# Optimization experiments

Hardware: AMD Instinct MI355X
Metric: run time of the kernel (lower is better)

The kernel has to match this reference:

```python
import jax, jax.numpy as jnp
import numpy as np
from jax import lax

B, T, U, H, INNER, V = 4, 200, 100, 320, 512, 1000
BLANK = 0


def setup_inputs() -> dict:
    key = jax.random.key(0)
    ks = jax.random.split(key, 8)
    enc_state = jax.random.normal(ks[0], (B, T, H), dtype=jnp.float32)
    dec_state = jax.random.normal(ks[1], (B, U + 1, H), dtype=jnp.float32)
    tokens = jax.random.randint(ks[2], (B, U), 1, V, dtype=jnp.int32)
    output_length = jnp.full((B,), T, dtype=jnp.int32)
    tokens_length = jnp.full((B,), U, dtype=jnp.int32)
    s1 = 1.0 / np.sqrt(2 * H)
    s2 = 1.0 / np.sqrt(INNER)
    W1 = jax.random.uniform(ks[3], (2 * H, INNER), minval=-s1, maxval=s1, dtype=jnp.float32)
    b1 = jax.random.uniform(ks[4], (INNER,), minval=-s1, maxval=s1, dtype=jnp.float32)
    W2 = jax.random.uniform(ks[5], (INNER, V), minval=-s2, maxval=s2, dtype=jnp.float32)
    b2 = jax.random.uniform(ks[6], (V,), minval=-s2, maxval=s2, dtype=jnp.float32)
    return {"enc_state": enc_state, "dec_state": dec_state, "tokens": tokens,
            "output_length": output_length, "tokens_length": tokens_length,
            "W1": W1, "b1": b1, "W2": W2, "b2": b2}


def joint_logits(enc_state, dec_state, W1, b1, W2, b2):
    # concat joint: cat(enc[b,t], dec[b,u]) @ W1 == enc @ W1[:H] + dec @ W1[H:]
    h_enc = jnp.einsum('bth,hi->bti', enc_state, W1[:H])      # (B,T,INNER)
    h_dec = jnp.einsum('buh,hi->bui', dec_state, W1[H:])      # (B,U+1,INNER)
    h = jnp.tanh(h_enc[:, :, None, :] + h_dec[:, None, :, :] + b1)  # (B,T,U+1,INNER)
    return jnp.einsum('btui,iv->btuv', h, W2) + b2            # (B,T,U+1,V)


def rnnt_loss(log_probs, tokens, output_length, tokens_length):
    # log_probs: (B,T,U+1,V); tokens: (B,U) int
    Bn, Tn, U1, _ = log_probs.shape
    blank_lp = log_probs[..., BLANK]                           # (B,T,U+1)
    label_lp = jnp.take_along_axis(
        log_probs[:, :, :U1 - 1, :],
        tokens[:, None, :, None].astype(jnp.int32).repeat(Tn, axis=1),
        axis=-1)[..., 0]                                       # (B,T,U)

    # row t=0: alpha[0,u] = sum_{u'<u} label_lp[0,u']
    def row0_step(c, a):
        n = c + a
        return n, n
    init0 = jnp.zeros((Bn,), dtype=log_probs.dtype)
    _, rest0 = lax.scan(row0_step, init0, label_lp[:, 0, :].T)  # (U,B)
    alpha0 = jnp.concatenate([init0[None], rest0], axis=0).T    # (B,U+1)

    def t_step(alpha_prev, xs):
        blank_prev, label_t = xs                # (B,U+1), (B,U)
        b = alpha_prev + blank_prev             # blank transition from row t-1
        def u_step(c, inp):
            b_u, a_prev = inp
            n = jnp.logaddexp(b_u, c + a_prev)
            return n, n
        first = b[:, 0]
        _, rest = lax.scan(u_step, first, (b[:, 1:].T, label_t.T))
        alpha_t = jnp.concatenate([first[None], rest], axis=0).T
        return alpha_t, alpha_t

    xs = (blank_lp[:, :-1, :].transpose(1, 0, 2), label_lp[:, 1:, :].transpose(1, 0, 2))
    _, alphas = lax.scan(t_step, alpha0, xs)                    # (T-1,B,U+1)
    alpha = jnp.concatenate([alpha0[None], alphas], axis=0).transpose(1, 0, 2)  # (B,T,U+1)

    bidx = jnp.arange(Bn)
    t_idx = output_length - 1
    u_idx = tokens_length
    ll = alpha[bidx, t_idx, u_idx] + blank_lp[bidx, t_idx, u_idx]
    return -jnp.mean(ll)


def reference(enc_state, dec_state, tokens, output_length, tokens_length, W1, b1, W2, b2):
    logits = joint_logits(enc_state, dec_state, W1, b1, W2, b2)
    log_probs = jax.nn.log_softmax(logits, axis=-1)
    return rnnt_loss(log_probs, tokens, output_length, tokens_length)
```

## Files before the change

### kernel.cpp

```cpp
#include <hip/hip_runtime.h>
#include <hip/hip_bf16.h>

#define T_DIM 200
#define U_DIM 100
#define U1    101
#define H_DIM 320
#define K_INNER 512
#define V_DIM 1000
#define B_DIM 4
#define ND 300
#define ROWS 48
#define CHUNK 8

typedef unsigned short ushort_t;
typedef unsigned char uchar_t;
typedef unsigned int uint32;
typedef long lfrag;

typedef float ffrag4 __attribute__((ext_vector_type(4)));

#define LOG2E   1.4426950408889634f
#define LOG2E16 (1.4426950408889634f * 0.0625f)
#define LN2     0.6931471805599453f

__device__ __forceinline__ float tanh_fast(float x) {
  float e = __expf(2.0f * x);
  return 1.0f - __fdividef(2.0f, e + 1.0f);
}

__device__ __forceinline__ uint2 pk_fp8x8(float t0, float t1, float t2, float t3,
                                          float t4, float t5, float t6, float t7) {
  uint2 r;
  r.x = (uint32)__builtin_amdgcn_cvt_pk_fp8_f32(t0, t1, 0, false);
  r.x = (uint32)__builtin_amdgcn_cvt_pk_fp8_f32(t2, t3, (int)r.x, true);
  r.y = (uint32)__builtin_amdgcn_cvt_pk_fp8_f32(t4, t5, 0, false);
  r.y = (uint32)__builtin_amdgcn_cvt_pk_fp8_f32(t6, t7, (int)r.y, true);
  return r;
}

__global__ __launch_bounds__(512)
void prep_kernel(const float* __restrict__ enc, const float* __restrict__ dec,
                 const float* __restrict__ W1, const float* __restrict__ W2,
                 float* __restrict__ hEnc, float* __restrict__ hDec,
                 uchar_t* __restrict__ W2f8)
{
  __shared__ union { float sIn[8][H_DIM]; float sW[8][1024]; } sh;
  const int tid = threadIdx.x;
  const int blk = blockIdx.x;

  if (blk < 151) {
    const float* inp; float* outp; int nRows, rowOff, b0;
    if (blk < 100) { inp = enc; outp = hEnc; nRows = B_DIM * T_DIM; rowOff = 0;     b0 = blk; }
    else           { inp = dec; outp = hDec; nRows = B_DIM * U1;    rowOff = H_DIM; b0 = blk - 100; }
    const int r0 = b0 * 8;
    for (int i = tid; i < 8 * H_DIM; i += 512) {
      int r = i / H_DIM, k = i - r * H_DIM;
      int rr = r0 + r;
      sh.sIn[r][k] = (rr < nRows) ? inp[(size_t)rr * H_DIM + k] : 0.0f;
    }
    __syncthreads();
    const int c = tid;
    float acc[8];
#pragma unroll
    for (int r = 0; r < 8; ++r) acc[r] = 0.0f;
    const float* Wp = W1 + (size_t)rowOff * K_INNER + c;
    for (int k = 0; k < H_DIM; k += 4) {
      float w0 = Wp[(size_t)(k + 0) * K_INNER];
      float w1 = Wp[(size_t)(k + 1) * K_INNER];
      float w2 = Wp[(size_t)(k + 2) * K_INNER];
      float w3 = Wp[(size_t)(k + 3) * K_INNER];
#pragma unroll
      for (int r = 0; r < 8; ++r) {
        float4 s = *(const float4*)&sh.sIn[r][k];
        acc[r] = fmaf(s.w, w3, fmaf(s.z, w2, fmaf(s.y, w1, fmaf(s.x, w0, acc[r]))));
      }
    }
#pragma unroll
    for (int r = 0; r < 8; ++r) {
      int rr = r0 + r;
      if (rr < nRows) outp[(size_t)rr * K_INNER + c] = acc[r];
    }
  } else {
    const int kc = blk - 151;
    for (int i = tid; i < 8 * 1024; i += 512) {
      int r = i >> 10, n = i & 1023;
      sh.sW[r][n] = (n < V_DIM) ? W2[(size_t)(kc * 8 + r) * V_DIM + n] : 0.0f;
    }
    __syncthreads();
#pragma unroll
    for (int h = 0; h < 2; ++h) {
      int n = tid + h * 512;
      uint2 pk = pk_fp8x8(sh.sW[0][n] * 16.f, sh.sW[1][n] * 16.f,
                          sh.sW[2][n] * 16.f, sh.sW[3][n] * 16.f,
                          sh.sW[4][n] * 16.f, sh.sW[5][n] * 16.f,
                          sh.sW[6][n] * 16.f, sh.sW[7][n] * 16.f);
      *(uint2*)&W2f8[((size_t)kc * 1024 + n) * 8] = pk;
    }
  }
}

__global__ __launch_bounds__(256, 3)
void joint_kernel(const float* __restrict__ hEnc, const float* __restrict__ hDec,
                  const float* __restrict__ b1, const uchar_t* __restrict__ W2f8,
                  const float* __restrict__ b2, const int* __restrict__ tokens,
                  float* __restrict__ pD)
{
  __shared__ union SU {
    uchar_t X[ROWS * K_INNER];
    float red[4][ROWS][4];
  } sh;

  const int tid = threadIdx.x;
  const int b  = blockIdx.z;
  const int t0 = blockIdx.y * 12;
  const int u0 = blockIdx.x * 4;

  for (int i = tid; i < ROWS * 64; i += 256) {
    const int row = i >> 6;
    const int G = i & 63;
    const int tcl = min(t0 + (row >> 2), T_DIM - 1);
    const int ucl = min(u0 + (row & 3), U1 - 1);
    const float* er = hEnc + (size_t)(b * T_DIM + tcl) * K_INNER;
    const float* dr = hDec + (size_t)(b * U1 + ucl) * K_INNER;
    const int k = G << 3;
    float4 e0 = *(const float4*)(er + k);
    float4 e1 = *(const float4*)(er + k + 4);
    float4 d0 = *(const float4*)(dr + k);
    float4 d1 = *(const float4*)(dr + k + 4);
    float4 c0 = *(const float4*)(b1 + k);
    float4 c1 = *(const float4*)(b1 + k + 4);
    uint2 pk = pk_fp8x8(tanh_fast(e0.x + d0.x + c0.x), tanh_fast(e0.y + d0.y + c0.y),
                        tanh_fast(e0.z + d0.z + c0.z), tanh_fast(e0.w + d0.w + c0.w),
                        tanh_fast(e1.x + d1.x + c1.x), tanh_fast(e1.y + d1.y + c1.y),
                        tanh_fast(e1.z + d1.z + c1.z), tanh_fast(e1.w + d1.w + c1.w));
    const int slot = (G + row) & 63;
    *(uint2*)&sh.X[row * K_INNER + (slot << 3)] = pk;
  }
  __syncthreads();

  const int wave = tid >> 6;
  const int lane = tid & 63;
  const int l15 = lane & 15;
  const int quad = lane >> 4;

  float sumexp[3][4], labelA[3][4], blankV[3][4];
#pragma unroll
  for (int i = 0; i < 3; ++i)
#pragma unroll
    for (int j = 0; j < 4; ++j) { sumexp[i][j] = 0.0f; labelA[i][j] = 0.0f; blankV[i][j] = 0.0f; }

  int tokv[4];
#pragma unroll
  for (int j = 0; j < 4; ++j)
    tokv[j] = (u0 + j < U_DIM) ? tokens[b * U_DIM + u0 + j] : -1;

#pragma unroll 1
  for (int ct = 0; ct < 4; ++ct) {
    const int nbase = ct * 256 + wave * 64;
    ffrag4 acc[3][4];
    ffrag4 zero4 = {0.0f, 0.0f, 0.0f, 0.0f};
#pragma unroll
    for (int rb = 0; rb < 3; ++rb)
#pragma unroll
      for (int cb = 0; cb < 4; ++cb) acc[rb][cb] = zero4;

#pragma unroll 4
    for (int ks = 0; ks < 16; ++ks) {
      const int kchunk = ks * 4 + quad;
      lfrag av[3];
#pragma unroll
      for (int rb = 0; rb < 3; ++rb) {
        const int m = rb * 16 + l15;
        const int slot = (kchunk + m) & 63;
        av[rb] = *(const lfrag*)&sh.X[m * K_INNER + (slot << 3)];
      }
      lfrag bv[4];
#pragma unroll
      for (int cb = 0; cb < 4; ++cb) {
        const int n = nbase + cb * 16 + l15;
        bv[cb] = *(const lfrag*)(W2f8 + ((size_t)kchunk * 1024 + n) * 8);
      }
#pragma unroll
      for (int rb = 0; rb < 3; ++rb)
#pragma unroll
        for (int cb = 0; cb < 4; ++cb)
          acc[rb][cb] = __builtin_amdgcn_mfma_f32_16x16x32_fp8_fp8(av[rb], bv[cb], acc[rb][cb], 0, 0, 0);
    }

#pragma unroll
    for (int cb = 0; cb < 4; ++cb) {
      const int v = nbase + cb * 16 + l15;
      const float b2v = (v < V_DIM) ? b2[v] : -1e30f;
      const float b2s = b2v * LOG2E;
#pragma unroll
      for (int rb = 0; rb < 3; ++rb)
#pragma unroll
        for (int reg = 0; reg < 4; ++reg) {
          float a = acc[rb][cb][reg];
          sumexp[rb][reg] += exp2f(fmaf(a, LOG2E16, b2s));
          labelA[rb][reg] += (v == tokv[reg]) ? a : 0.0f;
        }
    }
    if (nbase == 0) {
#pragma unroll
      for (int rb = 0; rb < 3; ++rb)
#pragma unroll
        for (int reg = 0; reg < 4; ++reg) blankV[rb][reg] = acc[rb][0][reg];
    }
  }

#pragma unroll
  for (int mask = 1; mask <= 8; mask <<= 1) {
#pragma unroll
    for (int rb = 0; rb < 3; ++rb)
#pragma unroll
      for (int reg = 0; reg < 4; ++reg) {
        sumexp[rb][reg] += __shfl_xor(sumexp[rb][reg], mask, 64);
        labelA[rb][reg] += __shfl_xor(labelA[rb][reg], mask, 64);
      }
  }

  __syncthreads();
  if (l15 == 0) {
#pragma unroll
    for (int rb = 0; rb < 3; ++rb)
#pragma unroll
      for (int reg = 0; reg < 4; ++reg) {
        int row = rb * 16 + quad * 4 + reg;
        sh.red[wave][row][0] = sumexp[rb][reg];
        sh.red[wave][row][1] = blankV[rb][reg];
        sh.red[wave][row][2] = labelA[rb][reg];
      }
  }
  __syncthreads();
  if (tid < ROWS) {
    float S  = sh.red[0][tid][0] + sh.red[1][tid][0] + sh.red[2][tid][0] + sh.red[3][tid][0];
    float Bl = sh.red[0][tid][1] + sh.red[1][tid][1] + sh.red[2][tid][1] + sh.red[3][tid][1];
    float Lb = sh.red[0][tid][2] + sh.red[1][tid][2] + sh.red[2][tid][2] + sh.red[3][tid][2];
    int t = t0 + (tid >> 2);
    int u = u0 + (tid & 3);
    if (t < T_DIM && u < U1) {
      float lse2 = __log2f(S);
      int tok = (u < U_DIM) ? tokens[b * U_DIM + u] : 0;
      int d = t + u;
      size_t idx = (((size_t)b * ND + d) * 128 + u) * 2;
      pD[idx]     = fmaf(Bl, LOG2E16, b2[0]   * LOG2E) - lse2;
      pD[idx + 1] = fmaf(Lb, LOG2E16, b2[tok] * LOG2E) - lse2;
    }
  }
}

__global__ __launch_bounds__(256)
void dp_kernel(const float* __restrict__ pD,
               const int* __restrict__ outLen, const int* __restrict__ tokLen,
               float* __restrict__ outLoss)
{
  __shared__ float sD[4][2][CHUNK * 256];
  __shared__ float llsh[B_DIM];
  const int tid = threadIdx.x;
  const int wv = tid >> 6;
  const int lane = tid & 63;
  const float* src = pD + (size_t)wv * ND * 256;
  const int tIdx = outLen[wv] - 1;
  const int uIdx = tokLen[wv];
  const int dStar = tIdx + uIdx;
  const float NEG = -1e30f;
  const float blkStar = src[((size_t)dStar * 128 + uIdx) * 2];

  float aE = (lane == 0) ? 0.0f : NEG;
  float aO = NEG;
  float ll2 = 0.0f;
  if (dStar == 0 && lane == 0) ll2 = blkStar;

  const int uE = 2 * lane;

#define ISSUE(c, buf)                                                         \
  {                                                                           \
    const float* g_ = src + (size_t)(c) * (CHUNK * 256);                      \
    float* l_ = &sD[wv][(buf)][0];                                            \
    _Pragma("unroll")                                                         \
    for (int j_ = 0; j_ < CHUNK; ++j_)                                        \
      __builtin_amdgcn_global_load_lds(                                       \
        (const __attribute__((address_space(1))) void*)(g_ + j_ * 256 + lane * 4), \
        (__attribute__((address_space(3))) void*)(l_ + j_ * 256), 16, 0, 0);  \
  }

  ISSUE(0, 0)
#pragma unroll 1
  for (int c = 0; c < 38; ++c) {
    if (c < 37) {
      ISSUE(c + 1, (c + 1) & 1)
      asm volatile("s_waitcnt vmcnt(8)" ::: "memory");
    } else {
      asm volatile("s_waitcnt vmcnt(0)" ::: "memory");
    }
    const float* buf = &sD[wv][c & 1][0];
#pragma unroll
    for (int j = 0; j < CHUNK; ++j) {
      const int d = c * CHUNK + 1 + j;
      float4 q = *(const float4*)&buf[j * 256 + uE * 2];
      float aO_up = __shfl_up(aO, 1, 64);
      if (lane == 0) aO_up = NEG;
      float labUp = __shfl_up(q.w, 1, 64);
      float bt0 = aE + q.x, lt0 = aO_up + labUp;
      float mx0 = fmaxf(bt0, lt0), mn0 = fminf(bt0, lt0);
      float r0 = mx0 + __log2f(1.0f + exp2f(mn0 - mx0));
      int te = d - uE;
      float nE = ((uE <= U_DIM) && (te >= 0) && (te < T_DIM)) ? r0 : NEG;
      float bt1 = aO + q.z, lt1 = aE + q.y;
      float mx1 = fmaxf(bt1, lt1), mn1 = fminf(bt1, lt1);
      float r1 = mx1 + __log2f(1.0f + exp2f(mn1 - mx1));
      int to = te - 1;
      float nO = ((uE + 1 <= U_DIM) && (to >= 0) && (to < T_DIM)) ? r1 : NEG;
      aE = nE; aO = nO;
      if (d == dStar) {
        if (uIdx == uE)          ll2 = nE + blkStar;
        else if (uIdx == uE + 1) ll2 = nO + blkStar;
      }
    }
  }
#undef ISSUE

#pragma unroll
  for (int mask = 1; mask < 64; mask <<= 1) ll2 += __shfl_xor(ll2, mask, 64);
  if (lane == 0) llsh[wv] = ll2;
  __syncthreads();
  if (tid == 0)
    outLoss[0] = -(llsh[0] + llsh[1] + llsh[2] + llsh[3]) * 0.25f * LN2;
}

extern "C" void kernel_launch(void* const* d_in, const int* in_sizes, int n_in,
                              void* d_out, int out_size, void* d_ws, size_t ws_size,
                              hipStream_t stream)
{
  const float* enc    = (const float*)d_in[0];
  const float* dec    = (const float*)d_in[1];
  const int*   tokens = (const int*)d_in[2];
  const int*   outLen = (const int*)d_in[3];
  const int*   tokLen = (const int*)d_in[4];
  const float* W1     = (const float*)d_in[5];
  const float* b1     = (const float*)d_in[6];
  const float* W2     = (const float*)d_in[7];
  const float* b2     = (const float*)d_in[8];
  float* out = (float*)d_out;

  char* ws = (char*)d_ws;
  float*   hEnc = (float*)(ws + 0);
  float*   hDec = (float*)(ws + 1638400);
  uchar_t* W2f8 = (uchar_t*)(ws + 2465792);
  float*   pD   = (float*)(ws + 2990080);

  prep_kernel<<<dim3(215), dim3(512), 0, stream>>>(enc, dec, W1, W2, hEnc, hDec, W2f8);
  joint_kernel<<<dim3(26, 17, B_DIM), dim3(256), 0, stream>>>(hEnc, hDec, b1, W2f8, b2, tokens, pD);
  dp_kernel<<<dim3(1), dim3(256), 0, stream>>>(pD, outLen, tokLen, out);
}
```

Measured before the change: 276.6 us.

## Pad LDS rows, strength-reduce loads, triple-buffer DP chunks, use DPP shifts

The joint kernel's XOR-swizzled fp8 activation tile in LDS becomes a row layout padded to a 520-byte pitch. This simplifies the A-fragment address math and keeps bank conflicts low. W2 fragment loads now use an incrementing pointer instead of recomputing the index every k-step. In the DP kernel, chunk staging moves from double to triple buffering with two chunks kept in flight, and the lane shift-up uses a DPP wave-shift instead of __shfl_up, which shortens the latency of the serial wavefront recurrence. The cost is extra LDS in the DP kernel and a few redundant loads of the last chunk at the tail.

New measurement: 265.8 us. 1.04x faster.

```diff
diff --git a/kernel.cpp b/kernel.cpp
--- a/kernel.cpp
+++ b/kernel.cpp
@@ -10,6 +10,7 @@
 #define B_DIM 4
 #define ND 300
 #define ROWS 48
+#define XPITCH 520
 #define CHUNK 8
 
 typedef unsigned short ushort_t;
@@ -36,6 +37,11 @@
   r.y = (uint32)__builtin_amdgcn_cvt_pk_fp8_f32(t4, t5, 0, false);
   r.y = (uint32)__builtin_amdgcn_cvt_pk_fp8_f32(t6, t7, (int)r.y, true);
   return r;
+}
+
+__device__ __forceinline__ float dpp_up1(float v, float oldv) {
+  return __int_as_float(__builtin_amdgcn_update_dpp(
+      __float_as_int(oldv), __float_as_int(v), 0x138, 0xf, 0xf, false));
 }
 
 __global__ __launch_bounds__(512)
@@ -106,7 +112,7 @@
                   float* __restrict__ pD)
 {
   __shared__ union SU {
-    uchar_t X[ROWS * K_INNER];
+    uchar_t X[ROWS * XPITCH];
     float red[4][ROWS][4];
   } sh;
 
@@ -133,8 +139,7 @@
                         tanh_fast(e0.z + d0.z + c0.z), tanh_fast(e0.w + d0.w + c0.w),
                         tanh_fast(e1.x + d1.x + c1.x), tanh_fast(e1.y + d1.y + c1.y),
                         tanh_fast(e1.z + d1.z + c1.z), tanh_fast(e1.w + d1.w + c1.w));
-    const int slot = (G + row) & 63;
-    *(uint2*)&sh.X[row * K_INNER + (slot << 3)] = pk;
+    *(uint2*)&sh.X[row * XPITCH + (G << 3)] = pk;
   }
   __syncthreads();
 
@@ -153,6 +158,8 @@
 #pragma unroll
   for (int j = 0; j < 4; ++j)
     tokv[j] = (u0 + j < U_DIM) ? tokens[b * U_DIM + u0 + j] : -1;
+
+  const uchar_t* aB = &sh.X[l15 * XPITCH + quad * 8];
 
 #pragma unroll 1
   for (int ct = 0; ct < 4; ++ct) {
@@ -164,22 +171,19 @@
 #pragma unroll
       for (int cb = 0; cb < 4; ++cb) acc[rb][cb] = zero4;
 
+    const uchar_t* bp = W2f8 + ((size_t)quad * 1024 + nbase + l15) * 8;
+
 #pragma unroll 4
     for (int ks = 0; ks < 16; ++ks) {
-      const int kchunk = ks * 4 + quad;
       lfrag av[3];
 #pragma unroll
-      for (int rb = 0; rb < 3; ++rb) {
-        const int m = rb * 16 + l15;
-        const int slot = (kchunk + m) & 63;
-        av[rb] = *(const lfrag*)&sh.X[m * K_INNER + (slot << 3)];
-      }
+      for (int rb = 0; rb < 3; ++rb)
+        av[rb] = *(const lfrag*)(aB + rb * (16 * XPITCH) + ks * 32);
       lfrag bv[4];
 #pragma unroll
-      for (int cb = 0; cb < 4; ++cb) {
-        const int n = nbase + cb * 16 + l15;
-        bv[cb] = *(const lfrag*)(W2f8 + ((size_t)kchunk * 1024 + n) * 8);
-      }
+      for (int cb = 0; cb < 4; ++cb)
+        bv[cb] = *(const lfrag*)(bp + cb * 128);
+      bp += 4 * 1024 * 8;
 #pragma unroll
       for (int rb = 0; rb < 3; ++rb)
 #pragma unroll
@@ -255,7 +259,7 @@
                const int* __restrict__ outLen, const int* __restrict__ tokLen,
                float* __restrict__ outLoss)
 {
-  __shared__ float sD[4][2][CHUNK * 256];
+  __shared__ float sD[4][3][CHUNK * 256];
   __shared__ float llsh[B_DIM];
   const int tid = threadIdx.x;
   const int wv = tid >> 6;
@@ -286,22 +290,18 @@
   }
 
   ISSUE(0, 0)
+  ISSUE(1, 1)
 #pragma unroll 1
   for (int c = 0; c < 38; ++c) {
-    if (c < 37) {
-      ISSUE(c + 1, (c + 1) & 1)
-      asm volatile("s_waitcnt vmcnt(8)" ::: "memory");
-    } else {
-      asm volatile("s_waitcnt vmcnt(0)" ::: "memory");
-    }
-    const float* buf = &sD[wv][c & 1][0];
+    { const int nc = c + 2; const int cc = nc <= 37 ? nc : 37; ISSUE(cc, nc % 3) }
+    asm volatile("s_waitcnt vmcnt(16)" ::: "memory");
+    const float* buf = &sD[wv][c % 3][0];
 #pragma unroll
     for (int j = 0; j < CHUNK; ++j) {
       const int d = c * CHUNK + 1 + j;
       float4 q = *(const float4*)&buf[j * 256 + uE * 2];
-      float aO_up = __shfl_up(aO, 1, 64);
-      if (lane == 0) aO_up = NEG;
-      float labUp = __shfl_up(q.w, 1, 64);
+      float aO_up = dpp_up1(aO, NEG);
+      float labUp = dpp_up1(q.w, NEG);
       float bt0 = aE + q.x, lt0 = aO_up + labUp;
       float mx0 = fmaxf(bt0, lt0), mn0 = fminf(bt0, lt0);
       float r0 = mx0 + __log2f(1.0f + exp2f(mn0 - mx0));
```
